# Kernel tuning notes

Measured on AMD Instinct MI355X. Metric: run time of the kernel, lower is better.

The kernel has to match this reference:

```python
import jax, jax.numpy as jnp
import numpy as np

B, N, IN_FT, OUT_FT = 1, 8192, 512, 256


def setup_inputs() -> dict:
    key = jax.random.key(0)
    k1, k2, k3, k4 = jax.random.split(key, 4)
    features = jax.random.normal(k1, (B, N, IN_FT), dtype=jnp.float32)
    adj = jax.random.uniform(k2, (B, N, N), dtype=jnp.float32)
    aug_adj1 = jax.random.uniform(k3, (B, N, N), dtype=jnp.float32)
    # Linear weight (xavier uniform), no bias on the Linear itself
    limit = float(np.sqrt(6.0 / (IN_FT + OUT_FT)))
    W = jax.random.uniform(k4, (OUT_FT, IN_FT), dtype=jnp.float32, minval=-limit, maxval=limit)
    bias = jnp.zeros((OUT_FT,), dtype=jnp.float32)  # GCN bias, filled 0
    prelu_a = jnp.full((1,), 0.25, dtype=jnp.float32)  # PReLU default slope
    return {"features": features, "adj": adj, "aug_adj1": aug_adj1,
            "W": W, "bias": bias, "prelu_a": prelu_a, "sparse": 0}


def _prelu(x, a):
    return jnp.where(x >= 0, x, a * x)


def _gcn(features, adj, W, bias, prelu_a):
    # Linear (no bias): [B,N,in] x [out,in]^T -> [B,N,out]
    seq_fts = jnp.einsum('bni,oi->bno', features, W)
    # Dense adjacency aggregation: bmm(adj, seq_fts)
    out = jnp.einsum('bnm,bmo->bno', adj, seq_fts) + bias
    return _prelu(out, prelu_a)


def reference(features, adj, aug_adj1, W, bias, prelu_a, sparse):
    # sparse flag is static (0 -> dense bmm path)
    h_0 = _gcn(features, adj, W, bias, prelu_a)
    h_1 = _gcn(features, aug_adj1, W, bias, prelu_a)
    return (h_0, h_1)
```

## Files before the change

### kernel.cpp

```cpp
#include <hip/hip_runtime.h>

#define NROW 8192
#define INF  512
#define OUTF 256
#define M_ELEM (NROW * OUTF)
#define NSTEP 32

typedef __bf16 v8bf __attribute__((ext_vector_type(8)));
typedef __bf16 v4bf __attribute__((ext_vector_type(4)));
typedef float  v4f  __attribute__((ext_vector_type(4)));

__device__ __forceinline__ v8bf cvt_bf8(v4f u0, v4f u1) {
  v8bf v;
  v[0]=(__bf16)u0[0]; v[1]=(__bf16)u0[1]; v[2]=(__bf16)u0[2]; v[3]=(__bf16)u0[3];
  v[4]=(__bf16)u1[0]; v[5]=(__bf16)u1[1]; v[6]=(__bf16)u1[2]; v[7]=(__bf16)u1[3];
  return v;
}

__global__ __launch_bounds__(256) void seq_fts_kernel(
    const float* __restrict__ feat, const float* __restrict__ W,
    __bf16* __restrict__ Bp) {
  const int tid  = threadIdx.x;
  const int lane = tid & 63, w = tid >> 6;
  const int llo  = lane & 15, lhi = lane >> 4;
  const int row0 = blockIdx.x * 64;
  const int col0 = w * 64;

  v4f acc[4][4] = {};
#pragma unroll 1
  for (int kb = 0; kb < INF / 32; ++kb) {
    const int kofs = kb * 32 + lhi * 8;
    v8bf a[4], b[4];
#pragma unroll
    for (int i = 0; i < 4; ++i) {
      const float* p = feat + (size_t)(row0 + i * 16 + llo) * INF + kofs;
      a[i] = cvt_bf8(*(const v4f*)p, *(const v4f*)(p + 4));
    }
#pragma unroll
    for (int i = 0; i < 4; ++i) {
      const float* p = W + (size_t)(col0 + i * 16 + llo) * INF + kofs;
      b[i] = cvt_bf8(*(const v4f*)p, *(const v4f*)(p + 4));
    }
#pragma unroll
    for (int ri = 0; ri < 4; ++ri)
#pragma unroll
      for (int ci = 0; ci < 4; ++ci)
        acc[ri][ci] = __builtin_amdgcn_mfma_f32_16x16x32_bf16(
            a[ri], b[ci], acc[ri][ci], 0, 0, 0);
  }
#pragma unroll
  for (int ri = 0; ri < 4; ++ri)
#pragma unroll
    for (int ci = 0; ci < 4; ++ci) {
      const int mf = row0 + ri * 16 + lhi * 4;
      const int o  = col0 + ci * 16 + llo;
      size_t e = (((size_t)(mf >> 5) * 16 + (o >> 4)) * 64 +
                  ((mf >> 3) & 3) * 16 + (o & 15)) * 8 + (mf & 7);
      v4bf v;
      v[0] = (__bf16)acc[ri][ci][0]; v[1] = (__bf16)acc[ri][ci][1];
      v[2] = (__bf16)acc[ri][ci][2]; v[3] = (__bf16)acc[ri][ci][3];
      *(v4bf*)(Bp + e) = v;
    }
}

__global__ __launch_bounds__(512, 1) void gcn_agg_kernel(
    const float* __restrict__ adjA, const float* __restrict__ adjB,
    const __bf16* __restrict__ Bp, const float* __restrict__ bias,
    const float* __restrict__ prelu_a, float* __restrict__ out) {
  const int tid  = threadIdx.x;
  const int lane = tid & 63, w = tid >> 6;
  const int llo  = lane & 15, lhi = lane >> 4;
  const int row0 = blockIdx.x * 64;
  const int z    = blockIdx.y;
  const float* __restrict__ adj = z ? adjB : adjA;

  __shared__ __align__(16) char LdsA[2][65536];

  v4f acc[4][2] = {};

  v4f areg[8];
  auto issue_a = [&](int t) {
#pragma unroll
    for (int i = 0; i < 8; ++i) {
      const int r = w * 8 + i;
      const float* src =
          adj + (size_t)(row0 + r) * NROW + t * 256 + (lane << 2);
      areg[i] = __builtin_nontemporal_load((const v4f*)src);
    }
  };
  auto write_a = [&](int buf) {
#pragma unroll
    for (int i = 0; i < 8; ++i) {
      const int r   = w * 8 + i;
      const int key = ((r & 15) << 1) | ((r >> 3) & 1);
      *(v4f*)(&LdsA[buf][r * 1024 + ((lane ^ key) << 4)]) = areg[i];
    }
  };

  const __bf16* __restrict__ Bpw = Bp + ((size_t)(w * 2) * 64 + lane) * 8;
  v8bf b[8][2];
  auto load_b_all = [&](int t) {
#pragma unroll
    for (int g = 0; g < 8; ++g)
#pragma unroll
      for (int ci = 0; ci < 2; ++ci)
        b[g][ci] = *(const v8bf*)(
            Bpw + ((size_t)((t * 8 + g) * 16 + ci)) * 512);
  };

  auto compute_g = [&](int buf, int kg) {
    const char* ab = &LdsA[buf][0];
    v8bf af[4];
#pragma unroll
    for (int rt = 0; rt < 4; ++rt) {
      const int r   = rt * 16 + llo;
      const int key = ((r & 15) << 1) | ((r >> 3) & 1);
      const char* base = ab + r * 1024;
      v4f u0 = *(const v4f*)(base + (((kg * 8 + lhi * 2    ) ^ key) << 4));
      v4f u1 = *(const v4f*)(base + (((kg * 8 + lhi * 2 + 1) ^ key) << 4));
      af[rt] = cvt_bf8(u0, u1);
    }
#pragma unroll
    for (int ci = 0; ci < 2; ++ci)
#pragma unroll
      for (int rt = 0; rt < 4; ++rt)
        acc[rt][ci] = __builtin_amdgcn_mfma_f32_16x16x32_bf16(
            af[rt], b[kg][ci], acc[rt][ci], 0, 0, 0);
  };

  issue_a(0);
  asm volatile("s_waitcnt vmcnt(0)" ::: "memory");
  write_a(0);
  asm volatile("s_waitcnt lgkmcnt(0)" ::: "memory");
  __builtin_amdgcn_s_barrier();

#pragma unroll 1
  for (int t = 0; t < NSTEP; ++t) {
    load_b_all(t);
    __builtin_amdgcn_sched_barrier(0);
    if (t + 1 < NSTEP) issue_a(t + 1);
    __builtin_amdgcn_sched_barrier(0);
#pragma unroll
    for (int kg = 0; kg < 8; ++kg)
      compute_g(t & 1, kg);
    __builtin_amdgcn_sched_barrier(0);
    if (t + 1 < NSTEP) {
      asm volatile("s_waitcnt vmcnt(0)" ::: "memory");
      write_a((t + 1) & 1);
      asm volatile("s_waitcnt lgkmcnt(0)" ::: "memory");
    }
    __builtin_amdgcn_s_barrier();
  }

  const float slope = prelu_a[0];
  float* __restrict__ outp = out + (size_t)z * M_ELEM;
#pragma unroll
  for (int ci = 0; ci < 2; ++ci) {
    const int o  = w * 32 + ci * 16 + llo;
    const float bs = bias[o];
#pragma unroll
    for (int rt = 0; rt < 4; ++rt) {
      const int m = row0 + rt * 16 + lhi * 4;
#pragma unroll
      for (int r = 0; r < 4; ++r) {
        float v = acc[rt][ci][r] + bs;
        outp[(size_t)(m + r) * OUTF + o] = v >= 0.f ? v : slope * v;
      }
    }
  }
}

extern "C" void kernel_launch(void* const* d_in, const int* in_sizes, int n_in,
                              void* d_out, int out_size, void* d_ws, size_t ws_size,
                              hipStream_t stream) {
  const float* feat = (const float*)d_in[0];
  const float* adj  = (const float*)d_in[1];
  const float* aug  = (const float*)d_in[2];
  const float* W    = (const float*)d_in[3];
  const float* bias = (const float*)d_in[4];
  const float* pa   = (const float*)d_in[5];
  float* out = (float*)d_out;
  __bf16* Bp = (__bf16*)d_ws;

  seq_fts_kernel<<<dim3(NROW / 64), 256, 0, stream>>>(feat, W, Bp);
  gcn_agg_kernel<<<dim3(NROW / 64, 2), 512, 0, stream>>>(
      adj, aug, Bp, bias, pa, out);
}
```

Measured before the change: 191.7 us.

## Stream adjacency tiles directly into LDS and double-buffer B fragments

Adjacency tiles now go straight from global memory into LDS through global_load_lds, with the XOR swizzle moved to the source address. This removes the register staging and the explicit LDS write step. The loop also prefetches tile t+2 while computing tile t, and splits the B fragment loads into two halves that are reissued one step ahead. The goal is to keep HBM loads in flight across compute and remove the full vmcnt(0) stalls, at the cost of careful vmcnt accounting and some redundant loads at the tail of the loop.

```diff
diff --git a/kernel.cpp b/kernel.cpp
--- a/kernel.cpp
+++ b/kernel.cpp
@@ -78,79 +78,93 @@
 
   v4f acc[4][2] = {};
 
-  v4f areg[8];
-  auto issue_a = [&](int t) {
-#pragma unroll
-    for (int i = 0; i < 8; ++i) {
-      const int r = w * 8 + i;
-      const float* src =
-          adj + (size_t)(row0 + r) * NROW + t * 256 + (lane << 2);
-      areg[i] = __builtin_nontemporal_load((const v4f*)src);
-    }
-  };
-  auto write_a = [&](int buf) {
+  auto stage_a = [&](int buf, int t) {
 #pragma unroll
     for (int i = 0; i < 8; ++i) {
       const int r   = w * 8 + i;
       const int key = ((r & 15) << 1) | ((r >> 3) & 1);
-      *(v4f*)(&LdsA[buf][r * 1024 + ((lane ^ key) << 4)]) = areg[i];
+      const float* src =
+          adj + (size_t)(row0 + r) * NROW + t * 256 + ((lane ^ key) << 2);
+      __builtin_amdgcn_global_load_lds(
+          (const __attribute__((address_space(1))) void*)src,
+          (__attribute__((address_space(3))) void*)(&LdsA[buf][r * 1024]),
+          16, 0, 2 );
     }
   };
 
   const __bf16* __restrict__ Bpw = Bp + ((size_t)(w * 2) * 64 + lane) * 8;
-  v8bf b[8][2];
-  auto load_b_all = [&](int t) {
-#pragma unroll
-    for (int g = 0; g < 8; ++g)
+  auto issue_b = [&](int half, v8bf (&b)[4][2]) {
+#pragma unroll
+    for (int g = 0; g < 4; ++g)
 #pragma unroll
       for (int ci = 0; ci < 2; ++ci)
         b[g][ci] = *(const v8bf*)(
-            Bpw + ((size_t)((t * 8 + g) * 16 + ci)) * 512);
+            Bpw + ((size_t)((half * 4 + g) * 16 + ci)) * 512);
   };
 
-  auto compute_g = [&](int buf, int kg) {
+  auto compute_half = [&](int buf, int h, v8bf (&b)[4][2]) {
     const char* ab = &LdsA[buf][0];
-    v8bf af[4];
-#pragma unroll
-    for (int rt = 0; rt < 4; ++rt) {
-      const int r   = rt * 16 + llo;
-      const int key = ((r & 15) << 1) | ((r >> 3) & 1);
-      const char* base = ab + r * 1024;
-      v4f u0 = *(const v4f*)(base + (((kg * 8 + lhi * 2    ) ^ key) << 4));
-      v4f u1 = *(const v4f*)(base + (((kg * 8 + lhi * 2 + 1) ^ key) << 4));
-      af[rt] = cvt_bf8(u0, u1);
-    }
-#pragma unroll
-    for (int ci = 0; ci < 2; ++ci)
-#pragma unroll
-      for (int rt = 0; rt < 4; ++rt)
-        acc[rt][ci] = __builtin_amdgcn_mfma_f32_16x16x32_bf16(
-            af[rt], b[kg][ci], acc[rt][ci], 0, 0, 0);
+#pragma unroll
+    for (int g = 0; g < 4; ++g) {
+      const int kg = h * 4 + g;
+      v8bf af[4];
+#pragma unroll
+      for (int rt = 0; rt < 4; ++rt) {
+        const int r   = rt * 16 + llo;
+        const int key = ((r & 15) << 1) | ((r >> 3) & 1);
+        const char* base = ab + r * 1024;
+        v4f u0 = *(const v4f*)(base + (((kg * 8 + lhi * 2    ) ^ key) << 4));
+        v4f u1 = *(const v4f*)(base + (((kg * 8 + lhi * 2 + 1) ^ key) << 4));
+        af[rt] = cvt_bf8(u0, u1);
+      }
+#pragma unroll
+      for (int ci = 0; ci < 2; ++ci)
+#pragma unroll
+        for (int rt = 0; rt < 4; ++rt)
+          acc[rt][ci] = __builtin_amdgcn_mfma_f32_16x16x32_bf16(
+              af[rt], b[g][ci], acc[rt][ci], 0, 0, 0);
+    }
   };
 
-  issue_a(0);
-  asm volatile("s_waitcnt vmcnt(0)" ::: "memory");
-  write_a(0);
-  asm volatile("s_waitcnt lgkmcnt(0)" ::: "memory");
+  v8bf bX[4][2], bY[4][2];
+
+  stage_a(0, 0);
+  issue_b(0, bX);
+  __builtin_amdgcn_sched_barrier(0);
+  issue_b(1, bY);
+  __builtin_amdgcn_sched_barrier(0);
+  stage_a(1, 1);
+  asm volatile("s_waitcnt vmcnt(24)" ::: "memory");
+  __builtin_amdgcn_sched_barrier(0);
   __builtin_amdgcn_s_barrier();
 
 #pragma unroll 1
   for (int t = 0; t < NSTEP; ++t) {
-    load_b_all(t);
-    __builtin_amdgcn_sched_barrier(0);
-    if (t + 1 < NSTEP) issue_a(t + 1);
-    __builtin_amdgcn_sched_barrier(0);
-#pragma unroll
-    for (int kg = 0; kg < 8; ++kg)
-      compute_g(t & 1, kg);
-    __builtin_amdgcn_sched_barrier(0);
-    if (t + 1 < NSTEP) {
-      asm volatile("s_waitcnt vmcnt(0)" ::: "memory");
-      write_a((t + 1) & 1);
-      asm volatile("s_waitcnt lgkmcnt(0)" ::: "memory");
-    }
+    const int p = t & 1;
+    compute_half(p, 0, bX);
+    __builtin_amdgcn_sched_barrier(0);
+    {
+      const int hb = (2 * t + 2 < 2 * NSTEP) ? 2 * t + 2 : 2 * NSTEP - 2;
+      issue_b(hb, bX);
+    }
+    __builtin_amdgcn_sched_barrier(0);
+    compute_half(p, 1, bY);
+    __builtin_amdgcn_sched_barrier(0);
+    {
+      const int hb = (2 * t + 3 < 2 * NSTEP) ? 2 * t + 3 : 2 * NSTEP - 1;
+      issue_b(hb, bY);
+    }
+    __builtin_amdgcn_sched_barrier(0);
+    __builtin_amdgcn_s_barrier();
+    {
+      const int ta = (t + 2 < NSTEP) ? t + 2 : NSTEP - 1;
+      stage_a(p, ta);
+    }
+    asm volatile("s_waitcnt vmcnt(24)" ::: "memory");
+    __builtin_amdgcn_sched_barrier(0);
     __builtin_amdgcn_s_barrier();
   }
+  asm volatile("s_waitcnt vmcnt(0)" ::: "memory");
 
   const float slope = prelu_a[0];
   float* __restrict__ outp = out + (size_t)z * M_ELEM;
```

Measured after the change: 169.3 us. 1.13x faster.
